# Kernel tuning notes

Hardware: AMD Instinct MI355X
Metric: run time of the kernel (lower is better)

The kernel has to match this reference:

```python
import jax, jax.numpy as jnp
import numpy as np

MARGIN = 5.0
VAR_FLOOR = 1e-4
BIG = 1e6


def setup_inputs() -> dict:
    key = jax.random.key(0)
    ks = jax.random.split(key, 8)
    B, D, R = 512, 768, 128
    C_new, C_old = 10, 100
    return {
        "features": jax.random.normal(ks[0], (B, D), jnp.float32),
        "labels": jax.random.randint(ks[1], (B,), 0, C_new),
        "new_class_ids": jnp.arange(C_new),
        "cur_means": jax.random.normal(ks[2], (C_new, D), jnp.float32),
        "cur_bases": jax.random.normal(ks[3], (C_new, D, R), jnp.float32),
        "cur_variances": jax.random.uniform(ks[4], (C_new, R + 1), jnp.float32),
        "calibrated_old_means": jax.random.normal(ks[5], (C_old, D), jnp.float32),
        "calibrated_old_bases": jax.random.normal(ks[6], (C_old, D, R), jnp.float32),
        "calibrated_old_variances": jax.random.uniform(ks[7], (C_old, R + 1), jnp.float32),
    }


def _geometry_distance_matrix(z, means, bases, variances):
    # z: [B,D], means: [C,D], bases: [C,D,R], variances: [C,R+1] -> [B,C]
    diff = z[:, None, :] - means[None, :, :]                    # [B,C,D]
    coeff = jnp.einsum('bcd,cdr->bcr', diff, bases)             # [B,C,R]
    eig = jnp.maximum(variances[:, :-1], VAR_FLOOR)             # [C,R]
    res = jnp.maximum(variances[:, -1], VAR_FLOOR)              # [C]
    parallel = jnp.sum(coeff * coeff / eig[None, :, :], axis=-1)  # [B,C]
    recon = jnp.einsum('bcr,cdr->bcd', coeff, bases)            # [B,C,D]
    residual_term = jnp.sum((diff - recon) ** 2, axis=-1) / res[None, :]
    dist = (parallel + residual_term) / z.shape[1]              # normalize_by_dim
    return jnp.nan_to_num(dist, nan=BIG, posinf=BIG, neginf=BIG)


def reference(features, labels, new_class_ids, cur_means, cur_bases, cur_variances,
              calibrated_old_means, calibrated_old_bases, calibrated_old_variances):
    z = jnp.nan_to_num(features, nan=0.0, posinf=0.0, neginf=0.0)  # [B,D]
    labels = labels.reshape(-1)

    own_all = _geometry_distance_matrix(z, cur_means, cur_bases, cur_variances)  # [B,C_new_total]
    old_all = _geometry_distance_matrix(z, calibrated_old_means, calibrated_old_bases,
                                        calibrated_old_variances)               # [B,C_old]
    old_min = jnp.min(old_all, axis=1)                                           # [B]

    # Per-new-class masks; union of class masks reproduces new_mask implicitly.
    masks = (labels[None, :] == new_class_ids[:, None]).astype(z.dtype)          # [K,B]
    counts = masks.sum(axis=1)                                                   # [K]
    denom = jnp.maximum(counts, 1.0)

    own_k = own_all[:, new_class_ids].T                                          # [K,B]
    hinge = jax.nn.relu(MARGIN + own_k - old_min[None, :])                       # [K,B]

    total_k = (hinge * masks).sum(axis=1) / denom
    own_k_mean = (own_k * masks).sum(axis=1) / denom
    old_k_mean = (old_min[None, :] * masks).sum(axis=1) / denom

    valid = (counts > 0).astype(z.dtype)
    n_valid = jnp.maximum(valid.sum(), 1.0)
    total = (total_k * valid).sum() / n_valid
    own = (own_k_mean * valid).sum() / n_valid
    old = (old_k_mean * valid).sum() / n_valid
    return jnp.stack([total, own, old])  # [total, own, old]
```

## Files before the change

### kernel.cpp

```cpp
#include <hip/hip_runtime.h>
#include <hip/hip_bf16.h>
#include <math.h>
#include <stdint.h>

#define B_N   512
#define D_N   768
#define R_N   128
#define C_NEW 10
#define C_OLD 100
#define C_TOT 110
#define MARGIN_F    5.0f
#define VAR_FLOOR_F 1e-4f
#define BIG_F       1e6f

typedef __bf16 bf16;
typedef __bf16 bf16x4 __attribute__((ext_vector_type(4)));
typedef __bf16 bf16x8 __attribute__((ext_vector_type(8)));
typedef float  f32x4  __attribute__((ext_vector_type(4)));

__device__ __forceinline__ float cleanf(float v) { return isfinite(v) ? v : 0.0f; }

__global__ __launch_bounds__(256)
void prep_zmu(const float* __restrict__ z,
              const float* __restrict__ cur_means, const float* __restrict__ old_means,
              bf16* __restrict__ zbf, float* __restrict__ znorm, float* __restrict__ munorm)
{
    const int tid = threadIdx.x, wave = tid >> 6, lane = tid & 63;
    __shared__ float s[4];

    if (blockIdx.x < 128) {
        const int b = blockIdx.x * 4 + wave;
        const float4* src = (const float4*)(z + (size_t)b * D_N);
        bf16x4* dst = (bf16x4*)(zbf + (size_t)b * D_N);
        float nrm = 0.f;
        #pragma unroll
        for (int i = 0; i < 3; ++i) {
            float4 v = src[lane + i * 64];
            v.x = cleanf(v.x); v.y = cleanf(v.y); v.z = cleanf(v.z); v.w = cleanf(v.w);
            nrm += v.x * v.x + v.y * v.y + v.z * v.z + v.w * v.w;
            bf16x4 w;
            w[0] = (bf16)v.x; w[1] = (bf16)v.y; w[2] = (bf16)v.z; w[3] = (bf16)v.w;
            dst[lane + i * 64] = w;
        }
        #pragma unroll
        for (int off = 32; off >= 1; off >>= 1) nrm += __shfl_xor(nrm, off, 64);
        if (lane == 0) znorm[b] = nrm;
        return;
    }

    const int c = blockIdx.x - 128;
    const float* mu = (c < C_NEW) ? cur_means + (size_t)c * D_N
                                  : old_means + (size_t)(c - C_NEW) * D_N;
    float p = 0.f;
    for (int d = tid; d < D_N; d += 256) p += mu[d] * mu[d];
    #pragma unroll
    for (int off = 32; off >= 1; off >>= 1) p += __shfl_xor(p, off, 64);
    if (lane == 0) s[wave] = p;
    __syncthreads();
    if (tid == 0) munorm[c] = s[0] + s[1] + s[2] + s[3];
}

__global__ __launch_bounds__(256)
void transpose_mc(const float* __restrict__ cur_bases, const float* __restrict__ old_bases,
                  const float* __restrict__ cur_means, const float* __restrict__ old_means,
                  bf16* __restrict__ basesT, float* __restrict__ m_c)
{
    const int dt = blockIdx.x, c = blockIdx.y;
    const float* Bc = (c < C_NEW) ? cur_bases + (size_t)c * D_N * R_N
                                  : old_bases + (size_t)(c - C_NEW) * D_N * R_N;
    const float* mu = (c < C_NEW) ? cur_means + (size_t)c * D_N
                                  : old_means + (size_t)(c - C_NEW) * D_N;
    __shared__ bf16 T[128][132];
    __shared__ float sMu[128];
    const int t = threadIdx.x;
    const int d0 = dt * 128;
    if (t < 128) sMu[t] = mu[d0 + t];

    #pragma unroll 4
    for (int it = 0; it < 16; ++it) {
        int q = it * 256 + t;
        int d = q >> 5, rr = (q & 31) * 4;
        float4 v = *(const float4*)(Bc + (size_t)(d0 + d) * R_N + rr);
        T[rr + 0][d] = (bf16)v.x;
        T[rr + 1][d] = (bf16)v.y;
        T[rr + 2][d] = (bf16)v.z;
        T[rr + 3][d] = (bf16)v.w;
    }
    __syncthreads();

    #pragma unroll 4
    for (int it = 0; it < 16; ++it) {
        int q = it * 256 + t;
        int r = q >> 5, dd = (q & 31) * 4;
        ushort4 w = *(const ushort4*)&T[r][dd];
        *(ushort4*)(basesT + (size_t)c * R_N * D_N + (size_t)r * D_N + d0 + dd) = w;
    }

    {
        int r = t & 127, dh = t >> 7;
        float p = 0.f;
        #pragma unroll 8
        for (int k = 0; k < 64; ++k) {
            int d = dh * 64 + k;
            p += sMu[d] * (float)T[r][d];
        }
        atomicAdd(&m_c[c * R_N + r], p);
    }
}

__global__ __launch_bounds__(256)
void gram(const bf16* __restrict__ basesT, bf16* __restrict__ G)
{
    const int hc = blockIdx.x, c = blockIdx.y;
    const bf16* Tc = basesT + (size_t)c * R_N * D_N;
    __shared__ bf16 sT[128][72];
    const int tid = threadIdx.x, wave = tid >> 6, lane = tid & 63;
    const int quad = lane >> 4, l15 = lane & 15;
    const int wr = (wave >> 1) * 64;
    const int wc = hc * 64 + (wave & 1) * 32;

    f32x4 acc[4][2];
    #pragma unroll
    for (int i = 0; i < 4; ++i)
        #pragma unroll
        for (int j = 0; j < 2; ++j) acc[i][j] = (f32x4)0.0f;

    for (int k0 = 0; k0 < D_N; k0 += 64) {
        __syncthreads();
        #pragma unroll
        for (int p = 0; p < 4; ++p) {
            int q = p * 256 + tid, row = q >> 3, u = q & 7;
            *(uint4*)(&sT[row][u * 8]) = *(const uint4*)(Tc + (size_t)row * D_N + k0 + u * 8);
        }
        __syncthreads();
        #pragma unroll
        for (int kk = 0; kk < 64; kk += 32) {
            bf16x8 af[4], bg[2];
            #pragma unroll
            for (int i = 0; i < 4; ++i) af[i] = *(const bf16x8*)(&sT[wr + 16 * i + l15][kk + quad * 8]);
            #pragma unroll
            for (int j = 0; j < 2; ++j) bg[j] = *(const bf16x8*)(&sT[wc + 16 * j + l15][kk + quad * 8]);
            #pragma unroll
            for (int i = 0; i < 4; ++i)
                #pragma unroll
                for (int j = 0; j < 2; ++j)
                    acc[i][j] = __builtin_amdgcn_mfma_f32_16x16x32_bf16(af[i], bg[j], acc[i][j], 0, 0, 0);
        }
    }
    #pragma unroll
    for (int i = 0; i < 4; ++i)
        #pragma unroll
        for (int j = 0; j < 2; ++j)
            #pragma unroll
            for (int reg = 0; reg < 4; ++reg) {
                int r = wr + 16 * i + quad * 4 + reg;
                int s = wc + 16 * j + l15;
                G[(size_t)c * 16384 + (size_t)r * 128 + s] = (bf16)acc[i][j][reg];
            }
}

#define PADC 136
#define SM_A   0
#define SM_B   18432
#define SM_G   0
#define SM_C   36864
#define SM_M   (36864 + 34816)
#define SM_INV (SM_M + 512)
#define SM_PAR (SM_INV + 512)
#define SM_CN  (SM_PAR + 512)
#define SM_Q   (SM_CN + 512)
#define SM_T2  (SM_Q + 512)
#define SM_MU  (SM_T2 + 3072)
#define SM_SZ  (SM_MU + 1536)

__global__ __launch_bounds__(256, 2)
void main_dist(const bf16* __restrict__ zbf, const bf16* __restrict__ basesT,
               const bf16* __restrict__ G, const float* __restrict__ m_c,
               const float* __restrict__ cur_vars, const float* __restrict__ old_vars,
               const float* __restrict__ cur_means, const float* __restrict__ old_means,
               const float* __restrict__ znorm, const float* __restrict__ munorm,
               float* __restrict__ gdist)
{
    const int mt = blockIdx.x, c = blockIdx.y;
    const int b0 = mt * 128;
    const float* vars = (c < C_NEW) ? cur_vars + (size_t)c * (R_N + 1)
                                    : old_vars + (size_t)(c - C_NEW) * (R_N + 1);
    const float* mu = (c < C_NEW) ? cur_means + (size_t)c * D_N
                                  : old_means + (size_t)(c - C_NEW) * D_N;
    __shared__ __align__(16) unsigned char smem[SM_SZ];
    bf16*  sA   = (bf16*)(smem + SM_A);
    bf16*  sB   = (bf16*)(smem + SM_B);
    bf16*  sG   = (bf16*)(smem + SM_G);
    bf16*  sC   = (bf16*)(smem + SM_C);
    float* sM   = (float*)(smem + SM_M);
    float* sInv = (float*)(smem + SM_INV);
    float* sPar = (float*)(smem + SM_PAR);
    float* sCn  = (float*)(smem + SM_CN);
    float* sQ   = (float*)(smem + SM_Q);
    float* sT2  = (float*)(smem + SM_T2);
    bf16*  sMuB = (bf16*)(smem + SM_MU);

    const int tid = threadIdx.x, wave = tid >> 6, lane = tid & 63;
    const int quad = lane >> 4, l15 = lane & 15;
    const int wr = (wave >> 1) * 64, wc = (wave & 1) * 64;

    if (tid < 128) {
        sM[tid]   = m_c[c * R_N + tid];
        sInv[tid] = 1.0f / fmaxf(vars[tid], VAR_FLOOR_F);
        sQ[tid]   = 0.0f;
    }
    for (int i = tid; i < D_N; i += 256) sMuB[i] = (bf16)mu[i];

    f32x4 acc1[4][4];
    #pragma unroll
    for (int i = 0; i < 4; ++i)
        #pragma unroll
        for (int j = 0; j < 4; ++j) acc1[i][j] = (f32x4)0.0f;
    float zd = 0.f;
    const int zrow = tid >> 1, zhalf = tid & 1;

    const bf16* Az = zbf + (size_t)b0 * D_N;
    const bf16* Bb = basesT + (size_t)c * R_N * D_N;
    for (int k0 = 0; k0 < D_N; k0 += 64) {
        __syncthreads();
        #pragma unroll
        for (int p = 0; p < 4; ++p) {
            int q = p * 256 + tid, row = q >> 3, u = q & 7;
            *(uint4*)(sA + row * 72 + u * 8) = *(const uint4*)(Az + (size_t)row * D_N + k0 + u * 8);
            *(uint4*)(sB + row * 72 + u * 8) = *(const uint4*)(Bb + (size_t)row * D_N + k0 + u * 8);
        }
        __syncthreads();
        #pragma unroll
        for (int kk = 0; kk < 64; kk += 32) {
            bf16x8 af[4], bg[4];
            #pragma unroll
            for (int i = 0; i < 4; ++i) af[i] = *(const bf16x8*)(sA + (wr + 16 * i + l15) * 72 + kk + quad * 8);
            #pragma unroll
            for (int j = 0; j < 4; ++j) bg[j] = *(const bf16x8*)(sB + (wc + 16 * j + l15) * 72 + kk + quad * 8);
            #pragma unroll
            for (int i = 0; i < 4; ++i)
                #pragma unroll
                for (int j = 0; j < 4; ++j)
                    acc1[i][j] = __builtin_amdgcn_mfma_f32_16x16x32_bf16(af[i], bg[j], acc1[i][j], 0, 0, 0);
        }
        {
            const bf16* zr = sA + zrow * 72 + zhalf * 32;
            const bf16* mr = sMuB + k0 + zhalf * 32;
            #pragma unroll
            for (int m = 0; m < 4; ++m) {
                bf16x8 a = *(const bf16x8*)(zr + m * 8);
                bf16x8 b = *(const bf16x8*)(mr + m * 8);
                #pragma unroll
                for (int e = 0; e < 8; ++e) zd += (float)a[e] * (float)b[e];
            }
        }
    }
    sT2[512 + tid] = zd;

    #pragma unroll
    for (int j = 0; j < 4; ++j) {
        float mcv = sM[wc + 16 * j + l15];
        #pragma unroll
        for (int i = 0; i < 4; ++i)
            #pragma unroll
            for (int reg = 0; reg < 4; ++reg) {
                float cv = acc1[i][j][reg] - mcv;
                acc1[i][j][reg] = cv;
                int row = wr + 16 * i + quad * 4 + reg;
                int col = wc + 16 * j + l15;
                sC[row * PADC + col] = (bf16)cv;
            }
    }
    __syncthreads();

    {
        int row = tid >> 1, half = tid & 1;
        float par = 0.f, cn = 0.f;
        #pragma unroll
        for (int m = 0; m < 8; ++m) {
            bf16x8 v = *(const bf16x8*)(sC + row * PADC + half * 64 + m * 8);
            #pragma unroll
            for (int e = 0; e < 8; ++e) {
                float f = (float)v[e];
                int col = half * 64 + m * 8 + e;
                cn  += f * f;
                par += f * f * sInv[col];
            }
        }
        sT2[tid] = par;
        sT2[256 + tid] = cn;
    }
    #pragma unroll
    for (int p = 0; p < 8; ++p) {
        int q = p * 256 + tid, s = q >> 4, u = q & 15;
        *(uint4*)(sG + s * PADC + u * 8) = *(const uint4*)(G + (size_t)c * 16384 + (size_t)s * 128 + u * 8);
    }
    __syncthreads();
    if (tid < 128) {
        sPar[tid] = sT2[tid * 2] + sT2[tid * 2 + 1];
        sCn[tid]  = sT2[256 + tid * 2] + sT2[256 + tid * 2 + 1];
    }

    f32x4 acc2[4][4];
    #pragma unroll
    for (int i = 0; i < 4; ++i)
        #pragma unroll
        for (int j = 0; j < 4; ++j) acc2[i][j] = (f32x4)0.0f;
    #pragma unroll
    for (int kc = 0; kc < 128; kc += 32) {
        bf16x8 af[4], bg[4];
        #pragma unroll
        for (int i = 0; i < 4; ++i) af[i] = *(const bf16x8*)(sC + (wr + 16 * i + l15) * PADC + kc + quad * 8);
        #pragma unroll
        for (int j = 0; j < 4; ++j) bg[j] = *(const bf16x8*)(sG + (wc + 16 * j + l15) * PADC + kc + quad * 8);
        #pragma unroll
        for (int i = 0; i < 4; ++i)
            #pragma unroll
            for (int j = 0; j < 4; ++j)
                acc2[i][j] = __builtin_amdgcn_mfma_f32_16x16x32_bf16(af[i], bg[j], acc2[i][j], 0, 0, 0);
    }

    #pragma unroll
    for (int i = 0; i < 4; ++i)
        #pragma unroll
        for (int reg = 0; reg < 4; ++reg) {
            float qp = 0.f;
            #pragma unroll
            for (int j = 0; j < 4; ++j) qp += acc2[i][j][reg] * acc1[i][j][reg];
            qp += __shfl_xor(qp, 1, 64);
            qp += __shfl_xor(qp, 2, 64);
            qp += __shfl_xor(qp, 4, 64);
            qp += __shfl_xor(qp, 8, 64);
            if (l15 == 0) atomicAdd(&sQ[wr + 16 * i + quad * 4 + reg], qp);
        }
    __syncthreads();

    if (tid < 128) {
        int b = b0 + tid;
        float zdot = sT2[512 + tid * 2] + sT2[512 + tid * 2 + 1];
        float nd2 = znorm[b] - 2.0f * zdot + munorm[c];
        float res = fmaxf(vars[R_N], VAR_FLOOR_F);
        float dist = (sPar[tid] + (nd2 - 2.0f * sCn[tid] + sQ[tid]) / res) / (float)D_N;
        if (!isfinite(dist)) dist = BIG_F;
        gdist[(size_t)b * C_TOT + c] = dist;
    }
}

__global__ __launch_bounds__(64)
void finalize_stage1(const float* __restrict__ gdist,
                     const int* __restrict__ labels,
                     const int* __restrict__ ncid,
                     float* __restrict__ acc)
{
    const int b = blockIdx.x * 64 + threadIdx.x;
    const float* row = gdist + (size_t)b * C_TOT;
    float mn = 3.4e38f;
    #pragma unroll
    for (int cc = C_NEW; cc < C_TOT; ++cc) mn = fminf(mn, row[cc]);
    const int lab = labels[b];
    #pragma unroll
    for (int k = 0; k < C_NEW; ++k) {
        if (lab == ncid[k]) {
            int col = min(max(ncid[k], 0), C_TOT - 1);
            float ow = row[col];
            atomicAdd(&acc[k * 4 + 0], 1.0f);
            atomicAdd(&acc[k * 4 + 1], fmaxf(0.0f, MARGIN_F + ow - mn));
            atomicAdd(&acc[k * 4 + 2], ow);
            atomicAdd(&acc[k * 4 + 3], mn);
        }
    }
}

__global__ __launch_bounds__(64)
void finalize_stage2(const float* __restrict__ acc, float* __restrict__ out)
{
    if (threadIdx.x == 0) {
        float total = 0.f, own = 0.f, old = 0.f, nv = 0.f;
        #pragma unroll
        for (int k = 0; k < C_NEW; ++k) {
            float cnt = acc[k * 4 + 0];
            float den = fmaxf(cnt, 1.0f);
            if (cnt > 0.f) {
                nv += 1.f;
                total += acc[k * 4 + 1] / den;
                own   += acc[k * 4 + 2] / den;
                old   += acc[k * 4 + 3] / den;
            }
        }
        float nvd = fmaxf(nv, 1.0f);
        out[0] = total / nvd;
        out[1] = own / nvd;
        out[2] = old / nvd;
    }
}

extern "C" void kernel_launch(void* const* d_in, const int* in_sizes, int n_in,
                              void* d_out, int out_size, void* d_ws, size_t ws_size,
                              hipStream_t stream)
{
    const float* features  = (const float*)d_in[0];
    const int*   labels    = (const int*)d_in[1];
    const int*   ncid      = (const int*)d_in[2];
    const float* cur_means = (const float*)d_in[3];
    const float* cur_bases = (const float*)d_in[4];
    const float* cur_vars  = (const float*)d_in[5];
    const float* old_means = (const float*)d_in[6];
    const float* old_bases = (const float*)d_in[7];
    const float* old_vars  = (const float*)d_in[8];

    unsigned char* ws = (unsigned char*)d_ws;
    float* gdist  = (float*)(ws + 0);
    bf16*  zbf    = (bf16*) (ws + 225280);
    float* znorm  = (float*)(ws + 1011712);
    float* munorm = (float*)(ws + 1013760);
    float* m_c    = (float*)(ws + 1014272);
    float* acc    = (float*)(ws + 1070592);
    bf16*  basesT = (bf16*) (ws + 1070848);
    bf16*  G      = (bf16*) (ws + 22697728);

    hipMemsetAsync(m_c, 0, 56320 + 256, stream);

    prep_zmu<<<dim3(128 + C_TOT), dim3(256), 0, stream>>>(features, cur_means, old_means,
                                                          zbf, znorm, munorm);
    transpose_mc<<<dim3(6, C_TOT), dim3(256), 0, stream>>>(cur_bases, old_bases,
                                                           cur_means, old_means,
                                                           basesT, m_c);
    gram<<<dim3(2, C_TOT), dim3(256), 0, stream>>>(basesT, G);
    main_dist<<<dim3(4, C_TOT), dim3(256), 0, stream>>>(zbf, basesT, G, m_c,
                                                        cur_vars, old_vars,
                                                        cur_means, old_means,
                                                        znorm, munorm, gdist);
    finalize_stage1<<<dim3(8), dim3(64), 0, stream>>>(gdist, labels, ncid, acc);
    finalize_stage2<<<dim3(1), dim3(64), 0, stream>>>(acc, (float*)d_out);
}
```

Measured before the change: 162.3 us.

## Fuse prep kernels, move mean-projection into gram, atomic-min old distances

Merges the z/mean-norm prep and the bases transpose into one launch, and replaces the padded transpose tile with an XOR-swizzled layout. The mean-times-basis projection m_c moves into the gram kernel so it no longer needs float atomics or a memset. main_dist now reduces the old-class minimum per sample with an order-preserving unsigned atomicMin instead of writing the full distance matrix. The two finalize kernels become a single block. The intent is to cut launch count, the memset and global traffic, at the cost of extra per-tile work in gram for hc==0 blocks and atomic contention on the per-sample minimum.

Measured after the change: 159.9 us. Within noise of the previous version (-1.5%).

```diff
diff --git a/kernel.cpp b/kernel.cpp
--- a/kernel.cpp
+++ b/kernel.cpp
@@ -20,16 +20,28 @@
 
 __device__ __forceinline__ float cleanf(float v) { return isfinite(v) ? v : 0.0f; }
 
+__device__ __forceinline__ unsigned encf(float f) {
+    unsigned u = __float_as_uint(f);
+    return (u & 0x80000000u) ? ~u : (u | 0x80000000u);
+}
+__device__ __forceinline__ float decf(unsigned u) {
+    return (u & 0x80000000u) ? __uint_as_float(u & 0x7fffffffu) : __uint_as_float(~u);
+}
+
 __global__ __launch_bounds__(256)
-void prep_zmu(const float* __restrict__ z,
-              const float* __restrict__ cur_means, const float* __restrict__ old_means,
-              bf16* __restrict__ zbf, float* __restrict__ znorm, float* __restrict__ munorm)
+void prep_fused(const float* __restrict__ z,
+                const float* __restrict__ cur_means, const float* __restrict__ old_means,
+                const float* __restrict__ cur_bases, const float* __restrict__ old_bases,
+                bf16* __restrict__ zbf, float* __restrict__ znorm, float* __restrict__ munorm,
+                bf16* __restrict__ basesT, unsigned* __restrict__ ominE)
 {
+    const int bid = blockIdx.x;
     const int tid = threadIdx.x, wave = tid >> 6, lane = tid & 63;
-    __shared__ float s[4];
-
-    if (blockIdx.x < 128) {
-        const int b = blockIdx.x * 4 + wave;
+    __shared__ bf16 T[128][128];
+    __shared__ float s4[4];
+
+    if (bid < 128) {
+        const int b = bid * 4 + wave;
         const float4* src = (const float4*)(z + (size_t)b * D_N);
         bf16x4* dst = (bf16x4*)(zbf + (size_t)b * D_N);
         float nrm = 0.f;
@@ -44,76 +56,77 @@
         }
         #pragma unroll
         for (int off = 32; off >= 1; off >>= 1) nrm += __shfl_xor(nrm, off, 64);
-        if (lane == 0) znorm[b] = nrm;
+        if (lane == 0) { znorm[b] = nrm; ominE[b] = 0xFFFFFFFFu; }
         return;
     }
 
-    const int c = blockIdx.x - 128;
-    const float* mu = (c < C_NEW) ? cur_means + (size_t)c * D_N
-                                  : old_means + (size_t)(c - C_NEW) * D_N;
-    float p = 0.f;
-    for (int d = tid; d < D_N; d += 256) p += mu[d] * mu[d];
-    #pragma unroll
-    for (int off = 32; off >= 1; off >>= 1) p += __shfl_xor(p, off, 64);
-    if (lane == 0) s[wave] = p;
-    __syncthreads();
-    if (tid == 0) munorm[c] = s[0] + s[1] + s[2] + s[3];
-}
-
-__global__ __launch_bounds__(256)
-void transpose_mc(const float* __restrict__ cur_bases, const float* __restrict__ old_bases,
-                  const float* __restrict__ cur_means, const float* __restrict__ old_means,
-                  bf16* __restrict__ basesT, float* __restrict__ m_c)
-{
-    const int dt = blockIdx.x, c = blockIdx.y;
+    if (bid < 128 + C_TOT) {
+        const int c = bid - 128;
+        const float* mu = (c < C_NEW) ? cur_means + (size_t)c * D_N
+                                      : old_means + (size_t)(c - C_NEW) * D_N;
+        float p = 0.f;
+        for (int d = tid; d < D_N; d += 256) p += mu[d] * mu[d];
+        #pragma unroll
+        for (int off = 32; off >= 1; off >>= 1) p += __shfl_xor(p, off, 64);
+        if (lane == 0) s4[wave] = p;
+        __syncthreads();
+        if (tid == 0) munorm[c] = s4[0] + s4[1] + s4[2] + s4[3];
+        return;
+    }
+
+    const int tb = bid - (128 + C_TOT);
+    const int dt = tb % 6, c = tb / 6;
     const float* Bc = (c < C_NEW) ? cur_bases + (size_t)c * D_N * R_N
                                   : old_bases + (size_t)(c - C_NEW) * D_N * R_N;
-    const float* mu = (c < C_NEW) ? cur_means + (size_t)c * D_N
-                                  : old_means + (size_t)(c - C_NEW) * D_N;
-    __shared__ bf16 T[128][132];
-    __shared__ float sMu[128];
-    const int t = threadIdx.x;
     const int d0 = dt * 128;
-    if (t < 128) sMu[t] = mu[d0 + t];
-
-    #pragma unroll 4
+    const int rg  = tid & 31;
+    const int dgb = tid >> 5;
+
+    #pragma unroll
+    for (int i = 0; i < 4; ++i) {
+        const int dg = i * 8 + dgb;
+        const float* src = Bc + (size_t)(d0 + dg * 4) * R_N + rg * 4;
+        float4 v0 = *(const float4*)(src);
+        float4 v1 = *(const float4*)(src + R_N);
+        float4 v2 = *(const float4*)(src + 2 * R_N);
+        float4 v3 = *(const float4*)(src + 3 * R_N);
+        const float* f0 = (const float*)&v0;
+        const float* f1 = (const float*)&v1;
+        const float* f2 = (const float*)&v2;
+        const float* f3 = (const float*)&v3;
+        #pragma unroll
+        for (int j = 0; j < 4; ++j) {
+            const int R = rg * 4 + j;
+            const int pc = dg ^ (R & 31);
+            bf16x4 w;
+            w[0] = (bf16)f0[j]; w[1] = (bf16)f1[j]; w[2] = (bf16)f2[j]; w[3] = (bf16)f3[j];
+            *(bf16x4*)(&T[R][pc * 4]) = w;
+        }
+    }
+    __syncthreads();
+
+    #pragma unroll
     for (int it = 0; it < 16; ++it) {
-        int q = it * 256 + t;
-        int d = q >> 5, rr = (q & 31) * 4;
-        float4 v = *(const float4*)(Bc + (size_t)(d0 + d) * R_N + rr);
-        T[rr + 0][d] = (bf16)v.x;
-        T[rr + 1][d] = (bf16)v.y;
-        T[rr + 2][d] = (bf16)v.z;
-        T[rr + 3][d] = (bf16)v.w;
-    }
-    __syncthreads();
-
-    #pragma unroll 4
-    for (int it = 0; it < 16; ++it) {
-        int q = it * 256 + t;
-        int r = q >> 5, dd = (q & 31) * 4;
-        ushort4 w = *(const ushort4*)&T[r][dd];
-        *(ushort4*)(basesT + (size_t)c * R_N * D_N + (size_t)r * D_N + d0 + dd) = w;
-    }
-
-    {
-        int r = t & 127, dh = t >> 7;
-        float p = 0.f;
-        #pragma unroll 8
-        for (int k = 0; k < 64; ++k) {
-            int d = dh * 64 + k;
-            p += sMu[d] * (float)T[r][d];
-        }
-        atomicAdd(&m_c[c * R_N + r], p);
+        const int q = it * 256 + tid;
+        const int r = q >> 5, u = q & 31;
+        const int pc = u ^ (r & 31);
+        ushort4 w = *(const ushort4*)(&T[r][pc * 4]);
+        *(ushort4*)(basesT + (size_t)c * R_N * D_N + (size_t)r * D_N + d0 + u * 4) = w;
     }
 }
 
 __global__ __launch_bounds__(256)
-void gram(const bf16* __restrict__ basesT, bf16* __restrict__ G)
+void gram(const bf16* __restrict__ basesT,
+          const float* __restrict__ cur_means, const float* __restrict__ old_means,
+          bf16* __restrict__ G, float* __restrict__ m_c)
 {
     const int hc = blockIdx.x, c = blockIdx.y;
     const bf16* Tc = basesT + (size_t)c * R_N * D_N;
+    const float* mu = (c < C_NEW) ? cur_means + (size_t)c * D_N
+                                  : old_means + (size_t)(c - C_NEW) * D_N;
     __shared__ bf16 sT[128][72];
+    __shared__ float sMuF[64];
+    __shared__ float sRed[256];
     const int tid = threadIdx.x, wave = tid >> 6, lane = tid & 63;
     const int quad = lane >> 4, l15 = lane & 15;
     const int wr = (wave >> 1) * 64;
@@ -124,6 +137,7 @@
     for (int i = 0; i < 4; ++i)
         #pragma unroll
         for (int j = 0; j < 2; ++j) acc[i][j] = (f32x4)0.0f;
+    float mAcc = 0.f;
 
     for (int k0 = 0; k0 < D_N; k0 += 64) {
         __syncthreads();
@@ -132,6 +146,7 @@
             int q = p * 256 + tid, row = q >> 3, u = q & 7;
             *(uint4*)(&sT[row][u * 8]) = *(const uint4*)(Tc + (size_t)row * D_N + k0 + u * 8);
         }
+        if (hc == 0 && tid < 64) sMuF[tid] = mu[k0 + tid];
         __syncthreads();
         #pragma unroll
         for (int kk = 0; kk < 64; kk += 32) {
@@ -146,6 +161,17 @@
                 for (int j = 0; j < 2; ++j)
                     acc[i][j] = __builtin_amdgcn_mfma_f32_16x16x32_bf16(af[i], bg[j], acc[i][j], 0, 0, 0);
         }
+        if (hc == 0) {
+            const int rrow = tid >> 1, hf = tid & 1;
+            const bf16* tr = &sT[rrow][hf * 32];
+            const float* mf = sMuF + hf * 32;
+            #pragma unroll
+            for (int m = 0; m < 4; ++m) {
+                bf16x8 v = *(const bf16x8*)(tr + m * 8);
+                #pragma unroll
+                for (int e = 0; e < 8; ++e) mAcc += (float)v[e] * mf[m * 8 + e];
+            }
+        }
     }
     #pragma unroll
     for (int i = 0; i < 4; ++i)
@@ -157,6 +183,9 @@
                 int s = wc + 16 * j + l15;
                 G[(size_t)c * 16384 + (size_t)r * 128 + s] = (bf16)acc[i][j][reg];
             }
+    sRed[tid] = mAcc;
+    __syncthreads();
+    if (hc == 0 && tid < 128) m_c[c * R_N + tid] = sRed[2 * tid] + sRed[2 * tid + 1];
 }
 
 #define PADC 136
@@ -179,7 +208,7 @@
                const float* __restrict__ cur_vars, const float* __restrict__ old_vars,
                const float* __restrict__ cur_means, const float* __restrict__ old_means,
                const float* __restrict__ znorm, const float* __restrict__ munorm,
-               float* __restrict__ gdist)
+               float* __restrict__ gdist, unsigned* __restrict__ ominE)
 {
     const int mt = blockIdx.x, c = blockIdx.y;
     const int b0 = mt * 128;
@@ -342,39 +371,44 @@
         float res = fmaxf(vars[R_N], VAR_FLOOR_F);
         float dist = (sPar[tid] + (nd2 - 2.0f * sCn[tid] + sQ[tid]) / res) / (float)D_N;
         if (!isfinite(dist)) dist = BIG_F;
-        gdist[(size_t)b * C_TOT + c] = dist;
-    }
-}
-
-__global__ __launch_bounds__(64)
-void finalize_stage1(const float* __restrict__ gdist,
-                     const int* __restrict__ labels,
-                     const int* __restrict__ ncid,
-                     float* __restrict__ acc)
+        if (c < C_NEW) {
+            gdist[(size_t)b * C_NEW + c] = dist;
+        } else {
+            atomicMin(ominE + b, encf(dist));
+        }
+    }
+}
+
+__global__ __launch_bounds__(512)
+void finalize(const float* __restrict__ gdist, const unsigned* __restrict__ ominE,
+              const int* __restrict__ labels, const int* __restrict__ ncid,
+              float* __restrict__ out)
 {
-    const int b = blockIdx.x * 64 + threadIdx.x;
-    const float* row = gdist + (size_t)b * C_TOT;
-    float mn = 3.4e38f;
-    #pragma unroll
-    for (int cc = C_NEW; cc < C_TOT; ++cc) mn = fminf(mn, row[cc]);
-    const int lab = labels[b];
-    #pragma unroll
-    for (int k = 0; k < C_NEW; ++k) {
-        if (lab == ncid[k]) {
-            int col = min(max(ncid[k], 0), C_TOT - 1);
-            float ow = row[col];
-            atomicAdd(&acc[k * 4 + 0], 1.0f);
-            atomicAdd(&acc[k * 4 + 1], fmaxf(0.0f, MARGIN_F + ow - mn));
-            atomicAdd(&acc[k * 4 + 2], ow);
-            atomicAdd(&acc[k * 4 + 3], mn);
-        }
-    }
-}
-
-__global__ __launch_bounds__(64)
-void finalize_stage2(const float* __restrict__ acc, float* __restrict__ out)
-{
-    if (threadIdx.x == 0) {
+    __shared__ float acc[C_NEW * 4];
+    __shared__ int sNcid[C_NEW];
+    const int t = threadIdx.x;
+    if (t < C_NEW * 4) acc[t] = 0.f;
+    if (t < C_NEW) sNcid[t] = ncid[t];
+    __syncthreads();
+
+    {
+        float mn = decf(ominE[t]);
+        const int lab = labels[t];
+        #pragma unroll
+        for (int k = 0; k < C_NEW; ++k) {
+            if (lab == sNcid[k]) {
+                int col = min(max(sNcid[k], 0), C_NEW - 1);
+                float ow = gdist[(size_t)t * C_NEW + col];
+                atomicAdd(&acc[k * 4 + 0], 1.0f);
+                atomicAdd(&acc[k * 4 + 1], fmaxf(0.0f, MARGIN_F + ow - mn));
+                atomicAdd(&acc[k * 4 + 2], ow);
+                atomicAdd(&acc[k * 4 + 3], mn);
+            }
+        }
+    }
+    __syncthreads();
+
+    if (t == 0) {
         float total = 0.f, own = 0.f, old = 0.f, nv = 0.f;
         #pragma unroll
         for (int k = 0; k < C_NEW; ++k) {
@@ -409,27 +443,22 @@
     const float* old_vars  = (const float*)d_in[8];
 
     unsigned char* ws = (unsigned char*)d_ws;
-    float* gdist  = (float*)(ws + 0);
-    bf16*  zbf    = (bf16*) (ws + 225280);
-    float* znorm  = (float*)(ws + 1011712);
-    float* munorm = (float*)(ws + 1013760);
-    float* m_c    = (float*)(ws + 1014272);
-    float* acc    = (float*)(ws + 1070592);
-    bf16*  basesT = (bf16*) (ws + 1070848);
-    bf16*  G      = (bf16*) (ws + 22697728);
-
-    hipMemsetAsync(m_c, 0, 56320 + 256, stream);
-
-    prep_zmu<<<dim3(128 + C_TOT), dim3(256), 0, stream>>>(features, cur_means, old_means,
-                                                          zbf, znorm, munorm);
-    transpose_mc<<<dim3(6, C_TOT), dim3(256), 0, stream>>>(cur_bases, old_bases,
-                                                           cur_means, old_means,
-                                                           basesT, m_c);
-    gram<<<dim3(2, C_TOT), dim3(256), 0, stream>>>(basesT, G);
+    float*    gdist  = (float*)(ws + 0);
+    unsigned* ominE  = (unsigned*)(ws + 20480);
+    bf16*     zbf    = (bf16*) (ws + 22528);
+    float*    znorm  = (float*)(ws + 808960);
+    float*    munorm = (float*)(ws + 811008);
+    float*    m_c    = (float*)(ws + 811520);
+    bf16*     basesT = (bf16*) (ws + 867840);
+    bf16*     G      = (bf16*) (ws + 22494720);
+
+    prep_fused<<<dim3(128 + C_TOT + 6 * C_TOT), dim3(256), 0, stream>>>(
+        features, cur_means, old_means, cur_bases, old_bases,
+        zbf, znorm, munorm, basesT, ominE);
+    gram<<<dim3(2, C_TOT), dim3(256), 0, stream>>>(basesT, cur_means, old_means, G, m_c);
     main_dist<<<dim3(4, C_TOT), dim3(256), 0, stream>>>(zbf, basesT, G, m_c,
                                                         cur_vars, old_vars,
                                                         cur_means, old_means,
-                                                        znorm, munorm, gdist);
-    finalize_stage1<<<dim3(8), dim3(64), 0, stream>>>(gdist, labels, ncid, acc);
-    finalize_stage2<<<dim3(1), dim3(64), 0, stream>>>(acc, (float*)d_out);
-}
+                                                        znorm, munorm, gdist, ominE);
+    finalize<<<dim3(1), dim3(512), 0, stream>>>(gdist, ominE, labels, ncid, (float*)d_out);
+}
```
